# Kernel optimization log

Hardware: AMD Instinct MI355X
Metric: run time of the kernel (lower is better)

The kernel has to match this reference:

```python
import jax, jax.numpy as jnp
import numpy as np
from jax import lax

DN = ('NCH', 'OIH', 'NCH')

def conv1d(x, w, b, pad=0):
    y = lax.conv_general_dilated(x, w, window_strides=(1,), padding=[(pad, pad)], dimension_numbers=DN)
    return y + b[None, :, None]

def conv_transpose1d(x, w_torch, b):
    # torch ConvTranspose1d weight: [C_in, C_out, K]; equivalent to full conv with flipped kernel
    k = w_torch.shape[-1]
    w = jnp.flip(jnp.transpose(w_torch, (1, 0, 2)), axis=-1)  # [C_out, C_in, K]
    y = lax.conv_general_dilated(x, w, window_strides=(1,), padding=[(k - 1, k - 1)], dimension_numbers=DN)
    return y + b[None, :, None]

def converter(signal, w1, b1, w2, b2, wt, bt, w3, b3):
    h = jax.nn.relu(conv1d(signal, w1, b1))          # [B,10,n-2]
    h = jax.nn.relu(conv1d(h, w2, b2))               # [B,10,n-2]
    h = jax.nn.relu(conv_transpose1d(h, wt, bt))     # [B,10,n]
    h = jax.nn.sigmoid(conv1d(h, w3, b3))            # [B,2,n]
    return h

def setup_inputs() -> dict:
    key = jax.random.key(0)
    ks = jax.random.split(key, 12)
    B, C, n = 32, 128, 8192
    signal = jax.random.normal(ks[0], (B, C, n), dtype=jnp.float32)
    curr_diag = jax.random.uniform(ks[1], (B, n - 1), dtype=jnp.float32) + 0.5
    s = 0.1
    return {
        'signal': signal,
        'curr_diag': curr_diag,
        'index_diag': 1,
        'w1': jax.random.normal(ks[2], (10, C, 3), dtype=jnp.float32) * s,
        'b1': jax.random.normal(ks[3], (10,), dtype=jnp.float32) * s,
        'w2': jax.random.normal(ks[4], (10, 10, 1), dtype=jnp.float32) * s,
        'b2': jax.random.normal(ks[5], (10,), dtype=jnp.float32) * s,
        'wt': jax.random.normal(ks[6], (10, 10, 3), dtype=jnp.float32) * s,
        'bt': jax.random.normal(ks[7], (10,), dtype=jnp.float32) * s,
        'w3': jax.random.normal(ks[8], (2, 10, 1), dtype=jnp.float32) * s,
        'b3': jax.random.normal(ks[9], (2,), dtype=jnp.float32) * s,
        'const': jnp.float32(0.99),
    }

def reference(signal, curr_diag, index_diag, w1, b1, w2, b2, wt, bt, w3, b3, const):
    n = signal.shape[-1]
    lr = converter(signal, w1, b1, w2, b2, wt, bt, w3, b3)  # [B,2,n]
    left, right = lr[:, 0, :], lr[:, 1, :]
    # diag_len = n - index_diag; next diag has length diag_len - 1
    mass_in = curr_diag[:, 1:] * right[:, 1:n - index_diag]
    mass_in = mass_in + curr_diag[:, :-1] * left[:, index_diag:n - 1]
    mass_out = right[:, 0:n - index_diag - 1] + left[:, index_diag + 1:n]
    next_diag = const * mass_in / mass_out
    next_diag = jnp.log(next_diag)
    next_diag = next_diag - jnp.mean(next_diag)
    return next_diag
```

## Files before the change

### kernel.cpp

```cpp
#include <hip/hip_runtime.h>
#include <math.h>

#define B     32
#define CIN   128
#define NN    8192
#define N1    8190
#define CH    10
#define TOUT  252
#define NTILE 33

__global__ void k0_prep(const float* __restrict__ w1, float* __restrict__ wT)
{
    const int i = blockIdx.x * 256 + threadIdx.x;
    if (i < CIN * 32) {
        const int ci = i >> 5, r = i & 31;
        float v = 0.f;
        if (r < 30) {
            const int o = r / 3, k = r - o * 3;
            v = w1[(o * CIN + ci) * 3 + k];
        }
        wT[i] = v;
    }
}

__global__ __launch_bounds__(256, 4) void k_main(
    const float* __restrict__ sig, const float* __restrict__ wT,
    const float* __restrict__ b1, const float* __restrict__ w2, const float* __restrict__ b2,
    const float* __restrict__ wt, const float* __restrict__ bt,
    const float* __restrict__ w3, const float* __restrict__ b3,
    const float* __restrict__ cd, const float* __restrict__ cstp,
    float* __restrict__ outv, float* __restrict__ bsums)
{
    __shared__ float h2s[CH * 256];
    __shared__ float lsh[256], rsh[256];
    __shared__ float red[256];

    const int tid = threadIdx.x;
    const int b   = blockIdx.y;
    const int t0  = blockIdx.x * TOUT;
    const int g   = t0 - 2 + tid;
    const bool gvalid = (g >= 0) && (g < N1);
    const bool sh = (g > NN - 4);
    int gl = (g < 0) ? 0 : g;
    if (gl > NN - 4) gl = NN - 4;
    const float* sb = sig + (size_t)b * CIN * NN + gl;

    float y[CH];
#pragma unroll
    for (int o = 0; o < CH; ++o) y[o] = b1[o];

    for (int c = 0; c < 8; ++c) {
        float4 v[16];
#pragma unroll
        for (int j = 0; j < 16; ++j)
            v[j] = *(const float4*)(sb + (size_t)(c * 16 + j) * NN);

        const float* wbase = wT + c * 16 * 32;
#pragma unroll
        for (int j = 0; j < 16; ++j) {
            const float s0 = sh ? v[j].y : v[j].x;
            const float s1 = sh ? v[j].z : v[j].y;
            const float s2 = sh ? v[j].w : v[j].z;
            const float* wrow = wbase + j * 32;
#pragma unroll
            for (int o = 0; o < CH; ++o) {
                y[o] = fmaf(wrow[o * 3 + 0], s0, y[o]);
                y[o] = fmaf(wrow[o * 3 + 1], s1, y[o]);
                y[o] = fmaf(wrow[o * 3 + 2], s2, y[o]);
            }
        }
    }

#pragma unroll
    for (int o = 0; o < CH; ++o) y[o] = fmaxf(y[o], 0.f);
#pragma unroll
    for (int o = 0; o < CH; ++o) {
        float a = b2[o];
#pragma unroll
        for (int i = 0; i < CH; ++i) a = fmaf(w2[o * CH + i], y[i], a);
        h2s[o * 256 + tid] = gvalid ? fmaxf(a, 0.f) : 0.f;
    }
    __syncthreads();

    const int s = t0 + tid;
    if (tid < 254 && s < NN) {
        float acc[CH];
#pragma unroll
        for (int o = 0; o < CH; ++o) acc[o] = bt[o];
#pragma unroll
        for (int i = 0; i < CH; ++i) {
            const float a0 = h2s[i * 256 + tid];
            const float a1 = h2s[i * 256 + tid + 1];
            const float a2 = h2s[i * 256 + tid + 2];
            const float* wp = wt + i * CH * 3;
#pragma unroll
            for (int o = 0; o < CH; ++o) {
                acc[o] = fmaf(wp[o * 3 + 0], a2, acc[o]);
                acc[o] = fmaf(wp[o * 3 + 1], a1, acc[o]);
                acc[o] = fmaf(wp[o * 3 + 2], a0, acc[o]);
            }
        }
        float l = b3[0], r = b3[1];
#pragma unroll
        for (int o = 0; o < CH; ++o) {
            const float h3 = fmaxf(acc[o], 0.f);
            l = fmaf(w3[o],      h3, l);
            r = fmaf(w3[CH + o], h3, r);
        }
        lsh[tid] = 1.f / (1.f + __expf(-l));
        rsh[tid] = 1.f / (1.f + __expf(-r));
    }
    __syncthreads();

    float vlog = 0.f;
    const int t = t0 + tid;
    if (tid < TOUT && t < N1) {
        const float c0 = cd[(size_t)b * (NN - 1) + t];
        const float c1 = cd[(size_t)b * (NN - 1) + t + 1];
        const float mi = c1 * rsh[tid + 1] + c0 * lsh[tid + 1];
        const float mo = rsh[tid] + lsh[tid + 2];
        vlog = __logf(cstp[0] * mi / mo);
        outv[(size_t)b * N1 + t] = vlog;
    }

    red[tid] = vlog;
    __syncthreads();
#pragma unroll
    for (int st = 128; st > 0; st >>= 1) {
        if (tid < st) red[tid] += red[tid + st];
        __syncthreads();
    }
    if (tid == 0) bsums[blockIdx.y * NTILE + blockIdx.x] = red[0];
}

__global__ __launch_bounds__(256) void k3_meansub(
    const float* __restrict__ bsums, float* __restrict__ outv, int n)
{
    __shared__ float red[256];
    const int tid = threadIdx.x;
    float s = 0.f;
    for (int i = tid; i < NTILE * B; i += 256) s += bsums[i];
    red[tid] = s;
    __syncthreads();
#pragma unroll
    for (int st = 128; st > 0; st >>= 1) {
        if (tid < st) red[tid] += red[tid + st];
        __syncthreads();
    }
    const float mean = red[0] / (float)(B * N1);
    __syncthreads();
    const int i = blockIdx.x * 256 + tid;
    if (i < n) outv[i] -= mean;
}

extern "C" void kernel_launch(void* const* d_in, const int* in_sizes, int n_in,
                              void* d_out, int out_size, void* d_ws, size_t ws_size,
                              hipStream_t stream)
{
    const float* sig = (const float*)d_in[0];
    const float* cd  = (const float*)d_in[1];
    const float* w1  = (const float*)d_in[3];
    const float* b1  = (const float*)d_in[4];
    const float* w2  = (const float*)d_in[5];
    const float* b2  = (const float*)d_in[6];
    const float* wt  = (const float*)d_in[7];
    const float* bt  = (const float*)d_in[8];
    const float* w3  = (const float*)d_in[9];
    const float* b3  = (const float*)d_in[10];
    const float* cst = (const float*)d_in[11];

    float* outv = (float*)d_out;

    float* ws   = (float*)d_ws;
    float* wT   = ws;
    float* bsum = wT + CIN * 32;

    dim3 blk(256);

    k0_prep   <<<dim3(16), blk, 0, stream>>>(w1, wT);
    k_main    <<<dim3(NTILE, B), blk, 0, stream>>>(sig, wT, b1, w2, b2,
                                                   wt, bt, w3, b3, cd, cst, outv, bsum);
    k3_meansub<<<dim3((out_size + 255) / 256), blk, 0, stream>>>(bsum, outv, out_size);
}
```

Baseline: 243.4 us.

## Double-buffer signal loads in conv1 loop and use wavefront shuffle reduction

Restructures the 128-channel conv1 accumulation into 8-channel chunks with two register buffers, so the next chunk's global loads are issued before computing the current one. Scheduling barriers keep the compiler from reordering them. Also replaces the shared-memory tree reduction of block sums with wavefront shuffles plus a 4-entry shared array. The aim is to hide memory latency in this bandwidth-bound kernel, at the cost of extra register pressure under the occupancy launch bound.

```diff
diff --git a/kernel.cpp b/kernel.cpp
--- a/kernel.cpp
+++ b/kernel.cpp
@@ -23,6 +23,25 @@
     }
 }
 
+__device__ __forceinline__ void chunk8(const float4 (&v)[8], int cbase,
+                                       float (&y)[CH], bool sh,
+                                       const float* __restrict__ wTl)
+{
+#pragma unroll
+    for (int j = 0; j < 8; ++j) {
+        const float s0 = sh ? v[j].y : v[j].x;
+        const float s1 = sh ? v[j].z : v[j].y;
+        const float s2 = sh ? v[j].w : v[j].z;
+        const float* wrow = wTl + (cbase + j) * 32;
+#pragma unroll
+        for (int o = 0; o < CH; ++o) {
+            y[o] = fmaf(wrow[o * 3 + 0], s0, y[o]);
+            y[o] = fmaf(wrow[o * 3 + 1], s1, y[o]);
+            y[o] = fmaf(wrow[o * 3 + 2], s2, y[o]);
+        }
+    }
+}
+
 __global__ __launch_bounds__(256, 4) void k_main(
     const float* __restrict__ sig, const float* __restrict__ wT,
     const float* __restrict__ b1, const float* __restrict__ w2, const float* __restrict__ b2,
@@ -33,7 +52,7 @@
 {
     __shared__ float h2s[CH * 256];
     __shared__ float lsh[256], rsh[256];
-    __shared__ float red[256];
+    __shared__ float red[4];
 
     const int tid = threadIdx.x;
     const int b   = blockIdx.y;
@@ -43,32 +62,33 @@
     const bool sh = (g > NN - 4);
     int gl = (g < 0) ? 0 : g;
     if (gl > NN - 4) gl = NN - 4;
-    const float* sb = sig + (size_t)b * CIN * NN + gl;
+    const float* __restrict__ sb = sig + (size_t)b * CIN * NN + gl;
 
     float y[CH];
 #pragma unroll
     for (int o = 0; o < CH; ++o) y[o] = b1[o];
 
-    for (int c = 0; c < 8; ++c) {
-        float4 v[16];
-#pragma unroll
-        for (int j = 0; j < 16; ++j)
-            v[j] = *(const float4*)(sb + (size_t)(c * 16 + j) * NN);
-
-        const float* wbase = wT + c * 16 * 32;
-#pragma unroll
-        for (int j = 0; j < 16; ++j) {
-            const float s0 = sh ? v[j].y : v[j].x;
-            const float s1 = sh ? v[j].z : v[j].y;
-            const float s2 = sh ? v[j].w : v[j].z;
-            const float* wrow = wbase + j * 32;
-#pragma unroll
-            for (int o = 0; o < CH; ++o) {
-                y[o] = fmaf(wrow[o * 3 + 0], s0, y[o]);
-                y[o] = fmaf(wrow[o * 3 + 1], s1, y[o]);
-                y[o] = fmaf(wrow[o * 3 + 2], s2, y[o]);
-            }
-        }
+    float4 va[8], vb[8];
+#pragma unroll
+    for (int j = 0; j < 8; ++j)
+        va[j] = *(const float4*)(sb + (size_t)j * NN);
+
+    for (int c = 0; c < 16; c += 2) {
+        const float* sc1 = sb + (size_t)(c + 1) * 8 * NN;
+#pragma unroll
+        for (int j = 0; j < 8; ++j)
+            vb[j] = *(const float4*)(sc1 + (size_t)j * NN);
+        __builtin_amdgcn_sched_barrier(0);
+        chunk8(va, c * 8, y, sh, wT);
+
+        if (c < 14) {
+            const float* sc2 = sb + (size_t)(c + 2) * 8 * NN;
+#pragma unroll
+            for (int j = 0; j < 8; ++j)
+                va[j] = *(const float4*)(sc2 + (size_t)j * NN);
+        }
+        __builtin_amdgcn_sched_barrier(0);
+        chunk8(vb, c * 8 + 8, y, sh, wT);
     }
 
 #pragma unroll
@@ -123,14 +143,13 @@
         outv[(size_t)b * N1 + t] = vlog;
     }
 
-    red[tid] = vlog;
-    __syncthreads();
-#pragma unroll
-    for (int st = 128; st > 0; st >>= 1) {
-        if (tid < st) red[tid] += red[tid + st];
-        __syncthreads();
-    }
-    if (tid == 0) bsums[blockIdx.y * NTILE + blockIdx.x] = red[0];
+    float vs = vlog;
+#pragma unroll
+    for (int off = 32; off > 0; off >>= 1) vs += __shfl_down(vs, off);
+    if ((tid & 63) == 0) red[tid >> 6] = vs;
+    __syncthreads();
+    if (tid == 0)
+        bsums[blockIdx.y * NTILE + blockIdx.x] = red[0] + red[1] + red[2] + red[3];
 }
 
 __global__ __launch_bounds__(256) void k3_meansub(
```

Result: slower. 280.5 us (+15.2%).

## Split input-channel reduction across two thread groups and use wave-shuffle block sum

Applied to the files above, without the earlier changes.

Doubles the block to 512 threads. Each 256-thread half now accumulates the first conv over 64 of the 128 input channels, and the partial sums are combined through shared memory before the pointwise conv. This raises the number of in-flight loads and waves per tile, to hide the latency of the memory-heavy channel loop. The block sum now uses wave shuffles plus an 8-entry shared array in place of the log-step shared-memory tree. In exchange, the upper half of the threads sits idle during the later stages, and the block uses more shared memory and registers, which may limit occupancy.

```diff
diff --git a/kernel.cpp b/kernel.cpp
--- a/kernel.cpp
+++ b/kernel.cpp
@@ -23,7 +23,7 @@
     }
 }
 
-__global__ __launch_bounds__(256, 4) void k_main(
+__global__ __launch_bounds__(512, 4) void k_main(
     const float* __restrict__ sig, const float* __restrict__ wT,
     const float* __restrict__ b1, const float* __restrict__ w2, const float* __restrict__ b2,
     const float* __restrict__ wt, const float* __restrict__ bt,
@@ -31,31 +31,35 @@
     const float* __restrict__ cd, const float* __restrict__ cstp,
     float* __restrict__ outv, float* __restrict__ bsums)
 {
+    __shared__ float ypart[CH * 256];
     __shared__ float h2s[CH * 256];
     __shared__ float lsh[256], rsh[256];
-    __shared__ float red[256];
+    __shared__ float red[8];
 
     const int tid = threadIdx.x;
+    const int grp = tid >> 8;
+    const int lid = tid & 255;
     const int b   = blockIdx.y;
     const int t0  = blockIdx.x * TOUT;
-    const int g   = t0 - 2 + tid;
+    const int g   = t0 - 2 + lid;
     const bool gvalid = (g >= 0) && (g < N1);
     const bool sh = (g > NN - 4);
     int gl = (g < 0) ? 0 : g;
     if (gl > NN - 4) gl = NN - 4;
-    const float* sb = sig + (size_t)b * CIN * NN + gl;
+    const float* __restrict__ sb =
+        sig + (size_t)b * CIN * NN + (size_t)grp * 64 * NN + gl;
 
     float y[CH];
 #pragma unroll
-    for (int o = 0; o < CH; ++o) y[o] = b1[o];
+    for (int o = 0; o < CH; ++o) y[o] = grp ? 0.f : b1[o];
 
-    for (int c = 0; c < 8; ++c) {
+    for (int c = 0; c < 4; ++c) {
         float4 v[16];
 #pragma unroll
         for (int j = 0; j < 16; ++j)
             v[j] = *(const float4*)(sb + (size_t)(c * 16 + j) * NN);
 
-        const float* wbase = wT + c * 16 * 32;
+        const float* wbase = wT + (grp * 64 + c * 16) * 32;
 #pragma unroll
         for (int j = 0; j < 16; ++j) {
             const float s0 = sh ? v[j].y : v[j].x;
@@ -71,14 +75,23 @@
         }
     }
 
+    if (grp == 1) {
 #pragma unroll
-    for (int o = 0; o < CH; ++o) y[o] = fmaxf(y[o], 0.f);
+        for (int o = 0; o < CH; ++o) ypart[o * 256 + lid] = y[o];
+    }
+    __syncthreads();
+
+    if (grp == 0) {
 #pragma unroll
-    for (int o = 0; o < CH; ++o) {
-        float a = b2[o];
+        for (int o = 0; o < CH; ++o)
+            y[o] = fmaxf(y[o] + ypart[o * 256 + lid], 0.f);
 #pragma unroll
-        for (int i = 0; i < CH; ++i) a = fmaf(w2[o * CH + i], y[i], a);
-        h2s[o * 256 + tid] = gvalid ? fmaxf(a, 0.f) : 0.f;
+        for (int o = 0; o < CH; ++o) {
+            float a = b2[o];
+#pragma unroll
+            for (int i = 0; i < CH; ++i) a = fmaf(w2[o * CH + i], y[i], a);
+            h2s[o * 256 + lid] = gvalid ? fmaxf(a, 0.f) : 0.f;
+        }
     }
     __syncthreads();
 
@@ -123,14 +136,17 @@
         outv[(size_t)b * N1 + t] = vlog;
     }
 
-    red[tid] = vlog;
+    float vs = vlog;
+#pragma unroll
+    for (int off = 32; off > 0; off >>= 1) vs += __shfl_down(vs, off);
+    if ((tid & 63) == 0) red[tid >> 6] = vs;
     __syncthreads();
+    if (tid == 0) {
+        float sgrand = 0.f;
 #pragma unroll
-    for (int st = 128; st > 0; st >>= 1) {
-        if (tid < st) red[tid] += red[tid + st];
-        __syncthreads();
+        for (int k = 0; k < 8; ++k) sgrand += red[k];
+        bsums[blockIdx.y * NTILE + blockIdx.x] = sgrand;
     }
-    if (tid == 0) bsums[blockIdx.y * NTILE + blockIdx.x] = red[0];
 }
 
 __global__ __launch_bounds__(256) void k3_meansub(
@@ -175,10 +191,8 @@
     float* wT   = ws;
     float* bsum = wT + CIN * 32;
 
-    dim3 blk(256);
-
-    k0_prep   <<<dim3(16), blk, 0, stream>>>(w1, wT);
-    k_main    <<<dim3(NTILE, B), blk, 0, stream>>>(sig, wT, b1, w2, b2,
-                                                   wt, bt, w3, b3, cd, cst, outv, bsum);
-    k3_meansub<<<dim3((out_size + 255) / 256), blk, 0, stream>>>(bsum, outv, out_size);
+    k0_prep   <<<dim3(16), dim3(256), 0, stream>>>(w1, wT);
+    k_main    <<<dim3(NTILE, B), dim3(512), 0, stream>>>(sig, wT, b1, w2, b2,
+                                                         wt, bt, w3, b3, cd, cst, outv, bsum);
+    k3_meansub<<<dim3((out_size + 255) / 256), dim3(256), 0, stream>>>(bsum, outv, out_size);
 }
```

New measurement: 384.6 us. +58.0%, slower.

## Double-buffer signal chunks into LDS via async global_load_lds

Applied to the files above, without the earlier changes.

Replaces per-thread float4 register loads of the input signal with asynchronous global-to-LDS copies, staging 8 channels per chunk into two alternating shared buffers so the load of the next chunk overlaps the conv1 FMAs on the current one. Each thread then reads its three taps from LDS, which removes the per-thread shifted-select edge logic and the overlapping redundant float4 reads. The block reduction is also switched from a shared-memory tree to wavefront shuffles. In exchange it adds about 17KB of LDS per block and a barrier per chunk, which may cut occupancy and add sync cost.

```diff
diff --git a/kernel.cpp b/kernel.cpp
--- a/kernel.cpp
+++ b/kernel.cpp
@@ -8,6 +8,9 @@
 #define CH    10
 #define TOUT  252
 #define NTILE 33
+#define COLS  264
+#define CPC   8
+#define NCHK  16
 
 __global__ void k0_prep(const float* __restrict__ w1, float* __restrict__ wT)
 {
@@ -23,6 +26,34 @@
     }
 }
 
+typedef __attribute__((address_space(1))) void g_void;
+typedef __attribute__((address_space(3))) void l_void;
+
+__device__ __forceinline__ void gld16(const float* g, float* l)
+{
+    __builtin_amdgcn_global_load_lds((g_void*)g, (l_void*)l, 16, 0, 0);
+}
+
+__device__ __forceinline__ void stage_chunk(const float* __restrict__ sigb, int c,
+                                            float* buf, int tid, int scol0)
+{
+    const float* rowbase = sigb + (size_t)(c * CPC) * NN;
+#pragma unroll
+    for (int k = 0; k < 2; ++k) {
+        const int i = k * 256 + tid;
+        const int row = (int)((unsigned)i / 66u);
+        int col = scol0 + (i - row * 66) * 4;
+        col = col < 0 ? 0 : (col > NN - 4 ? NN - 4 : col);
+        gld16(rowbase + (size_t)row * NN + col, buf + i * 4);
+    }
+    if (tid < 16) {
+        const int i = 512 + tid;
+        int col = scol0 + (i - 462) * 4;
+        col = col > NN - 4 ? NN - 4 : col;
+        gld16(rowbase + (size_t)7 * NN + col, buf + i * 4);
+    }
+}
+
 __global__ __launch_bounds__(256, 4) void k_main(
     const float* __restrict__ sig, const float* __restrict__ wT,
     const float* __restrict__ b1, const float* __restrict__ w2, const float* __restrict__ b2,
@@ -31,37 +62,39 @@
     const float* __restrict__ cd, const float* __restrict__ cstp,
     float* __restrict__ outv, float* __restrict__ bsums)
 {
+    __shared__ float bufA[CPC * COLS];
+    __shared__ float bufB[CPC * COLS];
     __shared__ float h2s[CH * 256];
     __shared__ float lsh[256], rsh[256];
-    __shared__ float red[256];
+    __shared__ float red[4];
 
     const int tid = threadIdx.x;
     const int b   = blockIdx.y;
     const int t0  = blockIdx.x * TOUT;
+    const int scol0 = t0 - 4;
     const int g   = t0 - 2 + tid;
     const bool gvalid = (g >= 0) && (g < N1);
-    const bool sh = (g > NN - 4);
-    int gl = (g < 0) ? 0 : g;
-    if (gl > NN - 4) gl = NN - 4;
-    const float* sb = sig + (size_t)b * CIN * NN + gl;
+    const float* __restrict__ sigb = sig + (size_t)b * CIN * NN;
 
     float y[CH];
 #pragma unroll
     for (int o = 0; o < CH; ++o) y[o] = b1[o];
 
-    for (int c = 0; c < 8; ++c) {
-        float4 v[16];
-#pragma unroll
-        for (int j = 0; j < 16; ++j)
-            v[j] = *(const float4*)(sb + (size_t)(c * 16 + j) * NN);
-
-        const float* wbase = wT + c * 16 * 32;
-#pragma unroll
-        for (int j = 0; j < 16; ++j) {
-            const float s0 = sh ? v[j].y : v[j].x;
-            const float s1 = sh ? v[j].z : v[j].y;
-            const float s2 = sh ? v[j].w : v[j].z;
-            const float* wrow = wbase + j * 32;
+    stage_chunk(sigb, 0, bufA, tid, scol0);
+    __syncthreads();
+
+    for (int c = 0; c < NCHK; ++c) {
+        float* cur = (c & 1) ? bufB : bufA;
+        float* nxt = (c & 1) ? bufA : bufB;
+        if (c < NCHK - 1) stage_chunk(sigb, c + 1, nxt, tid, scol0);
+
+        const float* bl = cur + tid + 2;
+#pragma unroll
+        for (int j = 0; j < CPC; ++j) {
+            const float s0 = bl[j * COLS + 0];
+            const float s1 = bl[j * COLS + 1];
+            const float s2 = bl[j * COLS + 2];
+            const float* wrow = wT + (c * CPC + j) * 32;
 #pragma unroll
             for (int o = 0; o < CH; ++o) {
                 y[o] = fmaf(wrow[o * 3 + 0], s0, y[o]);
@@ -69,6 +102,7 @@
                 y[o] = fmaf(wrow[o * 3 + 2], s2, y[o]);
             }
         }
+        __syncthreads();
     }
 
 #pragma unroll
@@ -123,14 +157,13 @@
         outv[(size_t)b * N1 + t] = vlog;
     }
 
-    red[tid] = vlog;
-    __syncthreads();
-#pragma unroll
-    for (int st = 128; st > 0; st >>= 1) {
-        if (tid < st) red[tid] += red[tid + st];
-        __syncthreads();
-    }
-    if (tid == 0) bsums[blockIdx.y * NTILE + blockIdx.x] = red[0];
+    float vs = vlog;
+#pragma unroll
+    for (int off = 32; off > 0; off >>= 1) vs += __shfl_down(vs, off);
+    if ((tid & 63) == 0) red[tid >> 6] = vs;
+    __syncthreads();
+    if (tid == 0)
+        bsums[blockIdx.y * NTILE + blockIdx.x] = red[0] + red[1] + red[2] + red[3];
 }
 
 __global__ __launch_bounds__(256) void k3_meansub(
@@ -175,10 +208,8 @@
     float* wT   = ws;
     float* bsum = wT + CIN * 32;
 
-    dim3 blk(256);
-
-    k0_prep   <<<dim3(16), blk, 0, stream>>>(w1, wT);
-    k_main    <<<dim3(NTILE, B), blk, 0, stream>>>(sig, wT, b1, w2, b2,
-                                                   wt, bt, w3, b3, cd, cst, outv, bsum);
-    k3_meansub<<<dim3((out_size + 255) / 256), blk, 0, stream>>>(bsum, outv, out_size);
-}
+    k0_prep   <<<dim3(16), dim3(256), 0, stream>>>(w1, wT);
+    k_main    <<<dim3(NTILE, B), dim3(256), 0, stream>>>(sig, wT, b1, w2, b2,
+                                                         wt, bt, w3, b3, cd, cst, outv, bsum);
+    k3_meansub<<<dim3((out_size + 255) / 256), dim3(256), 0, stream>>>(bsum, outv, out_size);
+}
```

Result: no change. 239.6 us (-1.5%).
